# Optimization experiments

Hardware: AMD Instinct MI355X
Metric: run time of the kernel (lower is better)

The kernel has to match this reference:

```python
import jax, jax.numpy as jnp
import numpy as np

N_NODES = 1024  # must equal 2*out_channels due to readout(x.T)
N_EDGES = 524288
IN_C, HID_C, OUT_C = 64, 128, 512
MLP_H = 64  # hidden width of EdgeConv MLP


def _linear_init(key, fan_in, fan_out):
    # xavier-normal-like init
    std = (2.0 / (fan_in + fan_out)) ** 0.5
    return jax.random.normal(key, (fan_in, fan_out), dtype=jnp.float32) * std


def setup_inputs() -> dict:
    key = jax.random.key(0)
    ks = jax.random.split(key, 8)
    x = jax.random.normal(ks[0], (N_NODES, IN_C), dtype=jnp.float32)
    edge_index = jax.random.randint(ks[1], (2, N_EDGES), 0, N_NODES, dtype=jnp.int64)
    # conv1 MLP: Linear(2*IN_C, 64) -> ReLU -> Linear(64, HID_C)
    W1 = _linear_init(ks[2], 2 * IN_C, MLP_H); b1 = jnp.zeros((MLP_H,), jnp.float32)
    W2 = _linear_init(ks[3], MLP_H, HID_C);    b2 = jnp.zeros((HID_C,), jnp.float32)
    # conv2 MLP: Linear(2*HID_C, 64) -> ReLU -> Linear(64, OUT_C)
    W3 = _linear_init(ks[4], 2 * HID_C, MLP_H); b3 = jnp.zeros((MLP_H,), jnp.float32)
    W4 = _linear_init(ks[5], MLP_H, OUT_C);     b4 = jnp.zeros((OUT_C,), jnp.float32)
    # readout: Linear(2*OUT_C, OUT_C) applied to x.T (requires N_NODES == 2*OUT_C)
    Wr = _linear_init(ks[6], 2 * OUT_C, OUT_C); br = jnp.zeros((OUT_C,), jnp.float32)
    return {"x": x, "edge_index": edge_index,
            "W1": W1, "b1": b1, "W2": W2, "b2": b2,
            "W3": W3, "b3": b3, "W4": W4, "b4": b4,
            "Wr": Wr, "br": br}


def _edge_conv(x, src, dst, Wa, ba, Wb, bb):
    # message: mlp(cat[x_i, x_j])  with i=target (dst), j=source (src)
    e = jnp.concatenate([x[dst], x[src]], axis=-1)          # [E, 2C]
    m = jnp.maximum(e @ Wa + ba, 0.0) @ Wb + bb             # [E, C_out]
    agg = jax.ops.segment_max(m, dst, num_segments=N_NODES)  # max-aggregate per target node
    # nodes with no incoming edges -> 0 (PyG fill behavior)
    return jnp.where(jnp.isneginf(agg), 0.0, agg)


def reference(x, edge_index, W1, b1, W2, b2, W3, b3, W4, b4, Wr, br):
    src = edge_index[0]
    dst = edge_index[1]
    h = _edge_conv(x, src, dst, W1, b1, W2, b2)   # [N, HID_C]
    h = _edge_conv(h, src, dst, W3, b3, W4, b4)   # [N, OUT_C]
    # readout on h.T: [OUT_C, N] @ [N(=2*OUT_C), OUT_C] -> [OUT_C, OUT_C]
    return h.T @ Wr + br
```

## Files before the change

kernel.cpp:

```cpp
#include <hip/hip_runtime.h>
#include <hip/hip_bf16.h>
#include <float.h>
#include <math.h>

#define N_NODES 1024
#define N_EDGES 524288
#define IN_C    64
#define HID_C   128
#define OUT_C   512
#define MLP_H   64
#define ADJ_WORDS 32
#define KSPLIT  8
#define KCHUNK  (N_NODES / KSPLIT)

typedef __attribute__((ext_vector_type(8))) short short8;
typedef __attribute__((ext_vector_type(4))) float f32x4;

static __device__ __forceinline__ unsigned short f2bf(float f) {
    __hip_bfloat16 h = __float2bfloat16(f);
    return __builtin_bit_cast(unsigned short, h);
}

static __device__ __forceinline__ void pack_w_one(
        const float* __restrict__ W, unsigned short* __restrict__ Wpk, int C, int idx) {
    int lane = idx & 63;
    int kf = (idx >> 6) & 1;
    int nt = idx >> 7;
    int kbase = kf * 32 + (lane >> 4) * 8;
    int c = nt * 16 + (lane & 15);
#pragma unroll
    for (int e = 0; e < 8; ++e)
        Wpk[idx * 8 + e] = f2bf(W[(kbase + e) * C + c]);
}

__global__ __launch_bounds__(256) void k_init(
        unsigned int* __restrict__ adj,
        const float* __restrict__ W2, unsigned short* __restrict__ Wpk1,
        const float* __restrict__ W4, unsigned short* __restrict__ Wpk2,
        const float* __restrict__ x, const float* __restrict__ W1,
        const float* __restrict__ b1,
        float* __restrict__ A1, float* __restrict__ B1) {
    __shared__ float xs[4][IN_C];
    const int b = blockIdx.x, tid = threadIdx.x;
    if (b < 128) {
        adj[b * 256 + tid] = 0u;
        return;
    }
    if (b < 132) { pack_w_one(W2, Wpk1, HID_C, (b - 128) * 256 + tid); return; }
    if (b < 148) { pack_w_one(W4, Wpk2, OUT_C, (b - 132) * 256 + tid); return; }
    const int sub = tid >> 6, t = tid & 63;
    const int n = (b - 148) * 4 + sub;
    xs[sub][t] = x[n * IN_C + t];
    __syncthreads();
    float a = b1[t], bb = 0.f;
#pragma unroll
    for (int k = 0; k < IN_C; ++k) {
        float xv = xs[sub][k];
        a = fmaf(xv, W1[k * MLP_H + t], a);
        bb = fmaf(xv, W1[(IN_C + k) * MLP_H + t], bb);
    }
    A1[n * MLP_H + t] = a;
    B1[n * MLP_H + t] = bb;
}

__global__ void k_build_adj(const int* __restrict__ ei, unsigned int* __restrict__ adj) {
    int e = blockIdx.x * blockDim.x + threadIdx.x;
    if (e >= N_EDGES) return;
    int src = ei[e];
    int dst = ei[N_EDGES + e];
    atomicOr(&adj[dst * ADJ_WORDS + (src >> 5)], 1u << (src & 31));
}

template <int NTILES, int C_TOTAL, int BATCH, int MINW, bool FUSEX>
__global__ __launch_bounds__(256, MINW) void k_conv_mfma(
        const unsigned int* __restrict__ adj,
        const float* __restrict__ Anode, const float* __restrict__ Bnode,
        const unsigned short* __restrict__ Wpk, const float* __restrict__ bias_g,
        float* __restrict__ outv,
        const float* __restrict__ W3, const float* __restrict__ b3,
        float* __restrict__ A2out, float* __restrict__ B2out) {
    __shared__ unsigned short list[N_NODES + 16];
    __shared__ short8 zbuf[2][BATCH][2][64];
    __shared__ float hrow[FUSEX ? HID_C : 1];
    __shared__ float xsum[FUSEX ? HID_C : 1];
    __shared__ int cnt;
    const int i = blockIdx.x;
    const int tid = threadIdx.x;
    const int lane = tid & 63;
    const int wave = tid >> 6;
    const int g = lane >> 4;
    const int r = lane & 15;

    short8 wfr[NTILES][2];
#pragma unroll
    for (int n = 0; n < NTILES; ++n) {
        int nt = wave * NTILES + n;
#pragma unroll
        for (int kf = 0; kf < 2; ++kf)
            wfr[n][kf] = ((const short8*)Wpk)[(nt * 2 + kf) * 64 + lane];
    }
    const f32x4* Ap = (const f32x4*)(Anode + i * MLP_H);
    f32x4 a0 = Ap[g * 2], a1 = Ap[g * 2 + 1], a2 = Ap[8 + g * 2], a3 = Ap[9 + g * 2];

    if (wave == 0) {
        unsigned int bits = (lane < ADJ_WORDS) ? adj[i * ADJ_WORDS + lane] : 0u;
        int c = __popc(bits);
        int pre = c;
#pragma unroll
        for (int d = 1; d < 64; d <<= 1) {
            int t = __shfl_up(pre, d);
            if (lane >= d) pre += t;
        }
        int total = __shfl(pre, 63);
        int pos = pre - c;
        while (bits) {
            int b = __ffs(bits) - 1;
            bits &= bits - 1;
            list[pos++] = (unsigned short)(lane * 32 + b);
        }
        if (lane == 0) cnt = total;
    }
    __syncthreads();
    const int deg = cnt;
    const int padded = (deg + 15) & ~15;
    for (int p = deg + tid; p < padded; p += 256) list[p] = list[0];

    float mx[NTILES];
#pragma unroll
    for (int n = 0; n < NTILES; ++n) mx[n] = -INFINITY;

    auto build = [&](int buf, int base_tile, int ntl) {
#pragma unroll
        for (int u = 0; u < BATCH / 4; ++u) {
            int tt = u * 4 + wave;
            if (tt < ntl) {
                int j = list[(base_tile + tt) * 16 + r];
                const f32x4* Bp = (const f32x4*)(Bnode + (size_t)j * MLP_H);
                f32x4 b0 = Bp[g * 2], b1 = Bp[g * 2 + 1], b2 = Bp[8 + g * 2], b3v = Bp[9 + g * 2];
                f32x4 s0 = a0 + b0, s1 = a1 + b1, s2 = a2 + b2, s3 = a3 + b3v;
                short8 z0, z1;
#pragma unroll
                for (int e = 0; e < 4; ++e) {
                    z0[e]     = (short)f2bf(fmaxf(s0[e], 0.f));
                    z0[e + 4] = (short)f2bf(fmaxf(s1[e], 0.f));
                    z1[e]     = (short)f2bf(fmaxf(s2[e], 0.f));
                    z1[e + 4] = (short)f2bf(fmaxf(s3[e], 0.f));
                }
                zbuf[buf][tt][0][lane] = z0;
                zbuf[buf][tt][1][lane] = z1;
            }
        }
    };

    const int ntiles_e = padded >> 4;
    const f32x4 zero = {0.f, 0.f, 0.f, 0.f};

    __syncthreads();
    build(0, 0, min(BATCH, ntiles_e));
    __syncthreads();

    int cur = 0;
    for (int b0 = 0; b0 < ntiles_e; b0 += BATCH) {
        int nb = min(BATCH, ntiles_e - b0);
        int nxt = b0 + BATCH;
        if (nxt < ntiles_e) build(cur ^ 1, nxt, min(BATCH, ntiles_e - nxt));
        __builtin_amdgcn_s_setprio(1);
        for (int tt = 0; tt < nb; ++tt) {
            short8 z0 = zbuf[cur][tt][0][lane];
            short8 z1 = zbuf[cur][tt][1][lane];
#pragma unroll
            for (int n = 0; n < NTILES; ++n) {
                f32x4 acc = __builtin_amdgcn_mfma_f32_16x16x32_bf16(z0, wfr[n][0], zero, 0, 0, 0);
                acc = __builtin_amdgcn_mfma_f32_16x16x32_bf16(z1, wfr[n][1], acc, 0, 0, 0);
                mx[n] = fmaxf(mx[n], fmaxf(fmaxf(acc[0], acc[1]), fmaxf(acc[2], acc[3])));
            }
        }
        __builtin_amdgcn_s_setprio(0);
        __syncthreads();
        cur ^= 1;
    }

#pragma unroll
    for (int n = 0; n < NTILES; ++n) {
        mx[n] = fmaxf(mx[n], __shfl_xor(mx[n], 16));
        mx[n] = fmaxf(mx[n], __shfl_xor(mx[n], 32));
    }
    if (lane < 16) {
#pragma unroll
        for (int n = 0; n < NTILES; ++n) {
            int c = (wave * NTILES + n) * 16 + lane;
            float hv = (deg == 0) ? 0.f : mx[n] + bias_g[c];
            if constexpr (FUSEX) hrow[c] = hv;
            else                 outv[i * C_TOTAL + c] = hv;
        }
    }

    if constexpr (FUSEX) {
        __syncthreads();
        const int c = tid & 63;
        const int half = (tid >> 6) & 1;
        const int ksel = tid >> 7;
        const float* wp = W3 + (half * 128 + ksel * 64) * MLP_H + c;
        float s = 0.f;
#pragma unroll
        for (int k = 0; k < 64; ++k)
            s = fmaf(hrow[ksel * 64 + k], wp[k * MLP_H], s);
        if (ksel) xsum[half * 64 + c] = s;
        __syncthreads();
        if (!ksel) {
            s += xsum[half * 64 + c];
            if (half == 0) A2out[i * MLP_H + c] = s + b3[c];
            else           B2out[i * MLP_H + c] = s;
        }
    }
}

__global__ __launch_bounds__(256) void k_readout_part(
        const float* __restrict__ h2, const float* __restrict__ Wr,
        float* __restrict__ partial) {
    __shared__ float As[64][64];
    __shared__ float Bs[64][64];
    const int bid = blockIdx.x;
    const int kc = bid >> 6;
    const int c0 = ((bid >> 3) & 7) * 64;
    const int o0 = (bid & 7) * 64;
    const int k0 = kc * KCHUNK;
    const int tid = threadIdx.x;
    const int tx = tid & 15, ty = tid >> 4;
    float acc[4][4] = {};
    for (int ks = 0; ks < KCHUNK; ks += 64) {
        for (int s = tid; s < 1024; s += 256) {
            int rr = s >> 4;
            int cq = (s & 15) * 4;
            *(float4*)&As[rr][cq] = *(const float4*)&h2[(k0 + ks + rr) * OUT_C + c0 + cq];
            *(float4*)&Bs[rr][cq] = *(const float4*)&Wr[(k0 + ks + rr) * OUT_C + o0 + cq];
        }
        __syncthreads();
#pragma unroll 16
        for (int kk = 0; kk < 64; ++kk) {
            float4 a = *(float4*)&As[kk][ty * 4];
            float4 b = *(float4*)&Bs[kk][tx * 4];
            acc[0][0] = fmaf(a.x, b.x, acc[0][0]); acc[0][1] = fmaf(a.x, b.y, acc[0][1]);
            acc[0][2] = fmaf(a.x, b.z, acc[0][2]); acc[0][3] = fmaf(a.x, b.w, acc[0][3]);
            acc[1][0] = fmaf(a.y, b.x, acc[1][0]); acc[1][1] = fmaf(a.y, b.y, acc[1][1]);
            acc[1][2] = fmaf(a.y, b.z, acc[1][2]); acc[1][3] = fmaf(a.y, b.w, acc[1][3]);
            acc[2][0] = fmaf(a.z, b.x, acc[2][0]); acc[2][1] = fmaf(a.z, b.y, acc[2][1]);
            acc[2][2] = fmaf(a.z, b.z, acc[2][2]); acc[2][3] = fmaf(a.z, b.w, acc[2][3]);
            acc[3][0] = fmaf(a.w, b.x, acc[3][0]); acc[3][1] = fmaf(a.w, b.y, acc[3][1]);
            acc[3][2] = fmaf(a.w, b.z, acc[3][2]); acc[3][3] = fmaf(a.w, b.w, acc[3][3]);
        }
        __syncthreads();
    }
    float* pb = partial + (size_t)kc * (OUT_C * OUT_C);
#pragma unroll
    for (int u = 0; u < 4; ++u) {
        float4 v = {acc[u][0], acc[u][1], acc[u][2], acc[u][3]};
        *(float4*)&pb[(c0 + ty * 4 + u) * OUT_C + o0 + tx * 4] = v;
    }
}

__global__ __launch_bounds__(256) void k_readout_reduce(
        const float* __restrict__ partial, const float* __restrict__ br,
        float* __restrict__ out) {
    int i = blockIdx.x * 256 + threadIdx.x;
    const float4* p4 = (const float4*)partial;
    float4 s = p4[i];
#pragma unroll
    for (int k = 1; k < KSPLIT; ++k) {
        float4 t = p4[i + k * 65536];
        s.x += t.x; s.y += t.y; s.z += t.z; s.w += t.w;
    }
    float4 b = ((const float4*)br)[i & 127];
    s.x += b.x; s.y += b.y; s.z += b.z; s.w += b.w;
    ((float4*)out)[i] = s;
}

extern "C" void kernel_launch(void* const* d_in, const int* in_sizes, int n_in,
                              void* d_out, int out_size, void* d_ws, size_t ws_size,
                              hipStream_t stream) {
    const float* x  = (const float*)d_in[0];
    const int*   ei = (const int*)d_in[1];
    const float* W1 = (const float*)d_in[2];
    const float* b1 = (const float*)d_in[3];
    const float* W2 = (const float*)d_in[4];
    const float* b2 = (const float*)d_in[5];
    const float* W3 = (const float*)d_in[6];
    const float* b3 = (const float*)d_in[7];
    const float* W4 = (const float*)d_in[8];
    const float* b4 = (const float*)d_in[9];
    const float* Wr = (const float*)d_in[10];
    const float* br = (const float*)d_in[11];
    float* out = (float*)d_out;

    char* ws = (char*)d_ws;
    unsigned int* adj = (unsigned int*)ws;
    float* A1 = (float*)(ws + 131072);
    float* B1 = (float*)(ws + 393216);
    float* A2 = (float*)(ws + 655360);
    float* B2 = (float*)(ws + 917504);
    float* h2 = (float*)(ws + 1179648);
    unsigned short* Wpk1 = (unsigned short*)(ws + 3276800);
    unsigned short* Wpk2 = (unsigned short*)(ws + 3293184);
    float* partial = (float*)(ws + 3358720);

    k_init<<<dim3(404), dim3(256), 0, stream>>>(adj, W2, Wpk1, W4, Wpk2,
                                                x, W1, b1, A1, B1);
    k_build_adj<<<dim3(N_EDGES / 256), dim3(256), 0, stream>>>(ei, adj);
    k_conv_mfma<2, HID_C, 8, 4, true><<<dim3(N_NODES), dim3(256), 0, stream>>>(
        adj, A1, B1, Wpk1, b2, nullptr, W3, b3, A2, B2);
    k_conv_mfma<8, OUT_C, 8, 4, false><<<dim3(N_NODES), dim3(256), 0, stream>>>(
        adj, A2, B2, Wpk2, b4, h2, nullptr, nullptr, nullptr, nullptr);
    k_readout_part<<<dim3(64 * KSPLIT), dim3(256), 0, stream>>>(h2, Wr, partial);
    k_readout_reduce<<<dim3(256), dim3(256), 0, stream>>>(partial, br, out);
}
```

Before: 170.8 us.

## Replicate adjacency bitmap to spread atomics and fuse split-K readout reduction

Edge atomicOr updates are spread across 8 replicated adjacency bitmaps chosen by block index, which cuts contention on hot words. The conv kernels then OR the copies together when loading a row. The readout reduction kernel is folded into the partial GEMM: the last split-K block for each tile, found through an atomic counter with fences, sums the partials and adds the bias. This trades extra zeroing and adjacency reads plus fence overhead for less atomic contention and one fewer kernel launch.

```diff
diff --git a/kernel.cpp b/kernel.cpp
--- a/kernel.cpp
+++ b/kernel.cpp
@@ -10,6 +10,8 @@
 #define OUT_C   512
 #define MLP_H   64
 #define ADJ_WORDS 32
+#define NCOPY   8
+#define ADJ_CSZ (N_NODES * ADJ_WORDS)
 #define KSPLIT  8
 #define KCHUNK  (N_NODES / KSPLIT)
 
@@ -39,28 +41,33 @@
         const float* __restrict__ W4, unsigned short* __restrict__ Wpk2,
         const float* __restrict__ x, const float* __restrict__ W1,
         const float* __restrict__ b1,
-        float* __restrict__ A1, float* __restrict__ B1) {
+        float* __restrict__ A1, float* __restrict__ B1,
+        unsigned int* __restrict__ tile_cnt) {
     __shared__ float xs[4][IN_C];
     const int b = blockIdx.x, tid = threadIdx.x;
-    if (b < 128) {
+    if (b < 1024) {
         adj[b * 256 + tid] = 0u;
         return;
     }
-    if (b < 132) { pack_w_one(W2, Wpk1, HID_C, (b - 128) * 256 + tid); return; }
-    if (b < 148) { pack_w_one(W4, Wpk2, OUT_C, (b - 132) * 256 + tid); return; }
-    const int sub = tid >> 6, t = tid & 63;
-    const int n = (b - 148) * 4 + sub;
-    xs[sub][t] = x[n * IN_C + t];
-    __syncthreads();
-    float a = b1[t], bb = 0.f;
-#pragma unroll
-    for (int k = 0; k < IN_C; ++k) {
-        float xv = xs[sub][k];
-        a = fmaf(xv, W1[k * MLP_H + t], a);
-        bb = fmaf(xv, W1[(IN_C + k) * MLP_H + t], bb);
-    }
-    A1[n * MLP_H + t] = a;
-    B1[n * MLP_H + t] = bb;
+    if (b < 1028) { pack_w_one(W2, Wpk1, HID_C, (b - 1024) * 256 + tid); return; }
+    if (b < 1044) { pack_w_one(W4, Wpk2, OUT_C, (b - 1028) * 256 + tid); return; }
+    if (b < 1300) {
+        const int sub = tid >> 6, t = tid & 63;
+        const int n = (b - 1044) * 4 + sub;
+        xs[sub][t] = x[n * IN_C + t];
+        __syncthreads();
+        float a = b1[t], bb = 0.f;
+#pragma unroll
+        for (int k = 0; k < IN_C; ++k) {
+            float xv = xs[sub][k];
+            a = fmaf(xv, W1[k * MLP_H + t], a);
+            bb = fmaf(xv, W1[(IN_C + k) * MLP_H + t], bb);
+        }
+        A1[n * MLP_H + t] = a;
+        B1[n * MLP_H + t] = bb;
+        return;
+    }
+    if (tid < 64) tile_cnt[tid] = 0u;
 }
 
 __global__ void k_build_adj(const int* __restrict__ ei, unsigned int* __restrict__ adj) {
@@ -68,7 +75,8 @@
     if (e >= N_EDGES) return;
     int src = ei[e];
     int dst = ei[N_EDGES + e];
-    atomicOr(&adj[dst * ADJ_WORDS + (src >> 5)], 1u << (src & 31));
+    unsigned int* base = adj + (blockIdx.x & (NCOPY - 1)) * ADJ_CSZ;
+    atomicOr(&base[dst * ADJ_WORDS + (src >> 5)], 1u << (src & 31));
 }
 
 template <int NTILES, int C_TOTAL, int BATCH, int MINW, bool FUSEX>
@@ -103,7 +111,12 @@
     f32x4 a0 = Ap[g * 2], a1 = Ap[g * 2 + 1], a2 = Ap[8 + g * 2], a3 = Ap[9 + g * 2];
 
     if (wave == 0) {
-        unsigned int bits = (lane < ADJ_WORDS) ? adj[i * ADJ_WORDS + lane] : 0u;
+        unsigned int bits = 0u;
+        if (lane < ADJ_WORDS) {
+            const unsigned int* ap = adj + i * ADJ_WORDS + lane;
+#pragma unroll
+            for (int c = 0; c < NCOPY; ++c) bits |= ap[c * ADJ_CSZ];
+        }
         int c = __popc(bits);
         int pre = c;
 #pragma unroll
@@ -215,15 +228,18 @@
     }
 }
 
-__global__ __launch_bounds__(256) void k_readout_part(
+__global__ __launch_bounds__(256) void k_readout(
         const float* __restrict__ h2, const float* __restrict__ Wr,
-        float* __restrict__ partial) {
+        const float* __restrict__ br, float* __restrict__ partial,
+        unsigned int* __restrict__ tile_cnt, float* __restrict__ out) {
     __shared__ float As[64][64];
     __shared__ float Bs[64][64];
+    __shared__ unsigned int prev;
     const int bid = blockIdx.x;
     const int kc = bid >> 6;
-    const int c0 = ((bid >> 3) & 7) * 64;
-    const int o0 = (bid & 7) * 64;
+    const int tile = bid & 63;
+    const int c0 = (tile >> 3) * 64;
+    const int o0 = (tile & 7) * 64;
     const int k0 = kc * KCHUNK;
     const int tid = threadIdx.x;
     const int tx = tid & 15, ty = tid >> 4;
@@ -257,22 +273,27 @@
         float4 v = {acc[u][0], acc[u][1], acc[u][2], acc[u][3]};
         *(float4*)&pb[(c0 + ty * 4 + u) * OUT_C + o0 + tx * 4] = v;
     }
-}
-
-__global__ __launch_bounds__(256) void k_readout_reduce(
-        const float* __restrict__ partial, const float* __restrict__ br,
-        float* __restrict__ out) {
-    int i = blockIdx.x * 256 + threadIdx.x;
-    const float4* p4 = (const float4*)partial;
-    float4 s = p4[i];
-#pragma unroll
-    for (int k = 1; k < KSPLIT; ++k) {
-        float4 t = p4[i + k * 65536];
-        s.x += t.x; s.y += t.y; s.z += t.z; s.w += t.w;
-    }
-    float4 b = ((const float4*)br)[i & 127];
-    s.x += b.x; s.y += b.y; s.z += b.z; s.w += b.w;
-    ((float4*)out)[i] = s;
+
+    __threadfence();
+    if (tid == 0) prev = atomicAdd(&tile_cnt[tile], 1u);
+    __syncthreads();
+    if (prev == KSPLIT - 1) {
+        __threadfence();
+        for (int s = tid; s < 1024; s += 256) {
+            int rr = s >> 4;
+            int cq = (s & 15) * 4;
+            int off = (c0 + rr) * OUT_C + o0 + cq;
+            float4 v = *(const float4*)&partial[off];
+#pragma unroll
+            for (int k = 1; k < KSPLIT; ++k) {
+                float4 t = *(const float4*)&partial[(size_t)k * (OUT_C * OUT_C) + off];
+                v.x += t.x; v.y += t.y; v.z += t.z; v.w += t.w;
+            }
+            const float4 b = *(const float4*)&br[o0 + cq];
+            v.x += b.x; v.y += b.y; v.z += b.z; v.w += b.w;
+            *(float4*)&out[off] = v;
+        }
+    }
 }
 
 extern "C" void kernel_launch(void* const* d_in, const int* in_sizes, int n_in,
@@ -294,22 +315,22 @@
 
     char* ws = (char*)d_ws;
     unsigned int* adj = (unsigned int*)ws;
-    float* A1 = (float*)(ws + 131072);
-    float* B1 = (float*)(ws + 393216);
-    float* A2 = (float*)(ws + 655360);
-    float* B2 = (float*)(ws + 917504);
-    float* h2 = (float*)(ws + 1179648);
-    unsigned short* Wpk1 = (unsigned short*)(ws + 3276800);
-    unsigned short* Wpk2 = (unsigned short*)(ws + 3293184);
-    float* partial = (float*)(ws + 3358720);
-
-    k_init<<<dim3(404), dim3(256), 0, stream>>>(adj, W2, Wpk1, W4, Wpk2,
-                                                x, W1, b1, A1, B1);
+    float* A1 = (float*)(ws + 1048576);
+    float* B1 = (float*)(ws + 1310720);
+    float* A2 = (float*)(ws + 1572864);
+    float* B2 = (float*)(ws + 1835008);
+    float* h2 = (float*)(ws + 2097152);
+    unsigned short* Wpk1 = (unsigned short*)(ws + 4194304);
+    unsigned short* Wpk2 = (unsigned short*)(ws + 4210688);
+    float* partial = (float*)(ws + 4276224);
+    unsigned int* tile_cnt = (unsigned int*)(ws + 12664832);
+
+    k_init<<<dim3(1301), dim3(256), 0, stream>>>(adj, W2, Wpk1, W4, Wpk2,
+                                                 x, W1, b1, A1, B1, tile_cnt);
     k_build_adj<<<dim3(N_EDGES / 256), dim3(256), 0, stream>>>(ei, adj);
     k_conv_mfma<2, HID_C, 8, 4, true><<<dim3(N_NODES), dim3(256), 0, stream>>>(
         adj, A1, B1, Wpk1, b2, nullptr, W3, b3, A2, B2);
     k_conv_mfma<8, OUT_C, 8, 4, false><<<dim3(N_NODES), dim3(256), 0, stream>>>(
         adj, A2, B2, Wpk2, b4, h2, nullptr, nullptr, nullptr, nullptr);
-    k_readout_part<<<dim3(64 * KSPLIT), dim3(256), 0, stream>>>(h2, Wr, partial);
-    k_readout_reduce<<<dim3(256), dim3(256), 0, stream>>>(partial, br, out);
-}
+    k_readout<<<dim3(64 * KSPLIT), dim3(256), 0, stream>>>(h2, Wr, br, partial, tile_cnt, out);
+}
```

Result: slower. 224.1 us (+31.2%).
